# Performance work log

Measured on AMD Instinct MI355X. Metric: run time of the kernel, lower is better.

Reference implementation:

```python
import jax, jax.numpy as jnp
import numpy as np

ALPHA = 0.5  # config_param['alpha']


def setup_inputs() -> dict:
    key = jax.random.key(0)
    ks = jax.random.split(key, 10)
    B, T, N, E, H = 64, 20, 8192, 128, 128
    # sparse multi-hot basket indicators
    x = (jax.random.uniform(ks[0], (B, T, N)) < 0.01).astype(jnp.float32)
    seq_len = jax.random.randint(ks[1], (B,), 1, T + 1)  # pack_padded requires >=1
    A = jax.random.uniform(ks[2], (N, N), dtype=jnp.float32) * 0.01  # dense item-item adjacency
    W1 = jax.random.normal(ks[3], (E, N), dtype=jnp.float32) * 0.02
    b1 = jnp.zeros((E,), jnp.float32)
    W2 = jax.random.normal(ks[4], (E, N), dtype=jnp.float32) * 0.02
    b2 = jnp.zeros((E,), jnp.float32)
    W_ih = jax.random.normal(ks[5], (4 * H, E), dtype=jnp.float32) * 0.05
    W_hh = jax.random.normal(ks[6], (4 * H, H), dtype=jnp.float32) * 0.05
    b_ih = jnp.zeros((4 * H,), jnp.float32)
    b_hh = jnp.zeros((4 * H,), jnp.float32)
    W_out = jax.random.normal(ks[7], (N, H), dtype=jnp.float32) * 0.02
    I_B = jnp.ones((N,), jnp.float32) / N  # item_probs-style bias init
    threshold = jnp.array([0.005], jnp.float32)  # adj_matrix.mean()
    return dict(x=x, seq_len=seq_len, A=A, W1=W1, b1=b1, W2=W2, b2=b2,
                W_ih=W_ih, W_hh=W_hh, b_ih=b_ih, b_hh=b_hh,
                W_out=W_out, I_B=I_B, threshold=threshold)


def reference(x, seq_len, A, W1, b1, W2, b2, W_ih, W_hh, b_ih, b_hh, W_out, I_B, threshold):
    B, T, N = x.shape
    H = W_hh.shape[1]
    xf = x.reshape(B * T, N)
    # two basket encoders, elementwise max combine (dropout = identity in eval)
    e1 = jax.nn.relu(xf @ W1.T + b1)
    e2 = jax.nn.relu(xf @ W2.T + b2)
    basket = jnp.maximum(e1, e2).reshape(B, T, -1)  # [B, T, E]

    # 1-layer LSTM (torch gate order i,f,g,o); packed variable-length seqs
    # emulated by freezing (h, c) once t >= seq_len, so h_n matches pack_padded.
    valid = jnp.arange(T)[:, None] < seq_len[None, :]  # [T, B]
    xs = basket.transpose(1, 0, 2)                     # [T, B, E]
    b = b_ih + b_hh

    def step(carry, inp):
        h, c = carry
        x_t, v = inp
        gates = x_t @ W_ih.T + h @ W_hh.T + b
        i, f, g, o = jnp.split(gates, 4, axis=-1)
        c_new = jax.nn.sigmoid(f) * c + jax.nn.sigmoid(i) * jnp.tanh(g)
        h_new = jax.nn.sigmoid(o) * jnp.tanh(c_new)
        m = v[:, None]
        return (jnp.where(m, h_new, h), jnp.where(m, c_new, c)), None

    h0 = jnp.zeros((B, H), x.dtype)
    c0 = jnp.zeros((B, H), x.dtype)
    (h_n, _), _ = jax.lax.scan(step, (h0, c0), (xs, valid))

    p = jax.nn.sigmoid(h_n @ W_out.T)  # [B, N]
    # mm(p, diag(relu(I_B))) is algebraically an elementwise scale
    predict = (1.0 - ALPHA) * p + ALPHA * (p * jax.nn.relu(I_B) + jax.nn.relu(p @ A))
    return predict
```

## Files before the change

kernel.cpp:

```cpp
#include <hip/hip_runtime.h>
#include <hip/hip_bf16.h>
#include <stdint.h>

#define B_ 64
#define T_ 20
#define N_ 8192
#define E_ 128
#define H_ 128
#define G4 512
#define SPLITK 16

typedef short bf16x8 __attribute__((ext_vector_type(8)));
typedef float f32x4 __attribute__((ext_vector_type(4)));

__device__ __forceinline__ float sigmoidf_(float x){ return 1.0f/(1.0f+expf(-x)); }

__device__ __forceinline__ unsigned short f2bf(float f){
  union { float f; uint32_t u; } v; v.f = f;
  uint32_t u = v.u;
  uint32_t r = (u + 0x7FFFu + ((u >> 16) & 1u)) >> 16;
  return (unsigned short)r;
}
__device__ __forceinline__ uint32_t pk2(float a, float b){
  return (uint32_t)f2bf(a) | ((uint32_t)f2bf(b) << 16);
}
__device__ __forceinline__ float bf2f(unsigned short s){
  union { uint32_t u; float f; } v; v.u = ((uint32_t)s) << 16; return v.f;
}

__global__ void k_transpose(const float* __restrict__ W1, const float* __restrict__ W2,
                            float* __restrict__ W12T){
  __shared__ float t1[128][33];
  __shared__ float t2[128][33];
  int n0 = blockIdx.x * 32;
  int tid = threadIdx.x;
  int nl = tid & 31, eg = tid >> 5;
  for (int i = 0; i < 16; i++){
    int e = eg * 16 + i;
    t1[e][nl] = W1[(size_t)e*N_ + n0 + nl];
    t2[e][nl] = W2[(size_t)e*N_ + n0 + nl];
  }
  __syncthreads();
  for (int n = 0; n < 32; n++){
    float v = (tid < 128) ? t1[tid][n] : t2[tid-128][n];
    W12T[(size_t)(n0+n)*256 + tid] = v;
  }
}

__global__ void k_mlpx(const float* __restrict__ x, const int* __restrict__ seq_len,
                       const float* __restrict__ W12T, const float* __restrict__ b1,
                       const float* __restrict__ b2, const float* __restrict__ W_ih,
                       const float* __restrict__ b_ih, const float* __restrict__ b_hh,
                       float* __restrict__ Xp){
  int bt = blockIdx.x;
  int b = bt / T_, t = bt % T_;
  if (t >= seq_len[b]) return;
  __shared__ int idxs[1024];
  __shared__ int cnt;
  __shared__ float e2s[128];
  __shared__ float bx[128];
  int tid = threadIdx.x;
  if (tid == 0) cnt = 0;
  __syncthreads();
  const float4* xr = (const float4*)(x + (size_t)bt * N_);
  for (int i = 0; i < 8; i++){
    float4 v = xr[i*256 + tid];
    int base = (i*256 + tid)*4;
    if (v.x != 0.f){ int q = atomicAdd(&cnt,1); idxs[q] = base;   }
    if (v.y != 0.f){ int q = atomicAdd(&cnt,1); idxs[q] = base+1; }
    if (v.z != 0.f){ int q = atomicAdd(&cnt,1); idxs[q] = base+2; }
    if (v.w != 0.f){ int q = atomicAdd(&cnt,1); idxs[q] = base+3; }
  }
  __syncthreads();
  int m = cnt; if (m > 1024) m = 1024;
  float acc = (tid < 128) ? b1[tid] : b2[tid-128];
  for (int i = 0; i < m; i++)
    acc += W12T[(size_t)idxs[i]*256 + tid];
  acc = fmaxf(acc, 0.f);
  if (tid >= 128) e2s[tid-128] = acc;
  __syncthreads();
  if (tid < 128) bx[tid] = fmaxf(acc, e2s[tid]);
  __syncthreads();
  #pragma unroll
  for (int half = 0; half < 2; half++){
    int j = half*256 + tid;
    const float4* wr = (const float4*)(W_ih + (size_t)j * E_);
    float s0 = b_ih[j] + b_hh[j], s1 = 0.f, s2 = 0.f, s3 = 0.f;
    #pragma unroll
    for (int k4 = 0; k4 < 32; k4 += 4){
      float4 w, h;
      w = wr[k4+0]; h = *(const float4*)&bx[k4*4+ 0]; s0 += w.x*h.x + w.y*h.y + w.z*h.z + w.w*h.w;
      w = wr[k4+1]; h = *(const float4*)&bx[k4*4+ 4]; s1 += w.x*h.x + w.y*h.y + w.z*h.z + w.w*h.w;
      w = wr[k4+2]; h = *(const float4*)&bx[k4*4+ 8]; s2 += w.x*h.x + w.y*h.y + w.z*h.z + w.w*h.w;
      w = wr[k4+3]; h = *(const float4*)&bx[k4*4+12]; s3 += w.x*h.x + w.y*h.y + w.z*h.z + w.w*h.w;
    }
    Xp[(size_t)bt*G4 + j] = (s0 + s1) + (s2 + s3);
  }
}

__global__ void __launch_bounds__(512, 2)
k_lstm(const int* __restrict__ seq_len, const float* __restrict__ Xp,
       const float* __restrict__ W_hh, float* __restrict__ hn){
  int b = blockIdx.x;
  int L = seq_len[b];
  int j = threadIdx.x;
  float4 whh[32];
  const float4* wr = (const float4*)(W_hh + (size_t)j * H_);
  #pragma unroll
  for (int k = 0; k < 32; k++) whh[k] = wr[k];
  __shared__ float hs[128];
  __shared__ float gs[512];
  if (j < 128) hs[j] = 0.f;
  float c = 0.f;
  __syncthreads();
  for (int t = 0; t < L; t++){
    float s0 = Xp[((size_t)b*T_ + t)*G4 + j], s1 = 0.f, s2 = 0.f, s3 = 0.f;
    #pragma unroll
    for (int k = 0; k < 32; k += 4){
      float4 w, h;
      w = whh[k+0]; h = *(const float4*)&hs[k*4+ 0]; s0 += w.x*h.x + w.y*h.y + w.z*h.z + w.w*h.w;
      w = whh[k+1]; h = *(const float4*)&hs[k*4+ 4]; s1 += w.x*h.x + w.y*h.y + w.z*h.z + w.w*h.w;
      w = whh[k+2]; h = *(const float4*)&hs[k*4+ 8]; s2 += w.x*h.x + w.y*h.y + w.z*h.z + w.w*h.w;
      w = whh[k+3]; h = *(const float4*)&hs[k*4+12]; s3 += w.x*h.x + w.y*h.y + w.z*h.z + w.w*h.w;
    }
    gs[j] = (s0 + s1) + (s2 + s3);
    __syncthreads();
    if (j < 128){
      float i_ = gs[j], f_ = gs[128+j], gg = gs[256+j], o_ = gs[384+j];
      c = sigmoidf_(f_)*c + sigmoidf_(i_)*tanhf(gg);
      hs[j] = sigmoidf_(o_)*tanhf(c);
    }
    __syncthreads();
  }
  if (j < 128) hn[(size_t)b*H_ + j] = hs[j];
}

__global__ void k_pout(const float* __restrict__ hn, const float* __restrict__ W_out,
                       unsigned short* __restrict__ pbf){
  __shared__ unsigned short hb[64*128];
  int tid = threadIdx.x;
  {
    int row = tid >> 2;
    int k16 = (tid & 3) * 32;
    const float4* hr = (const float4*)(hn + (size_t)row*H_ + k16);
    #pragma unroll
    for (int i = 0; i < 4; i++){
      float4 a = hr[i*2], bq = hr[i*2+1];
      uint4 u; u.x = pk2(a.x,a.y); u.y = pk2(a.z,a.w); u.z = pk2(bq.x,bq.y); u.w = pk2(bq.z,bq.w);
      int blk = (k16 >> 3) + i;
      *(uint4*)&hb[row*128 + ((blk ^ (row & 7)) * 8)] = u;
    }
  }
  __syncthreads();
  int w = tid >> 6, l = tid & 63;
  int n0 = blockIdx.x * 128;
  f32x4 acc[8];
  #pragma unroll
  for (int i = 0; i < 8; i++) acc[i] = (f32x4){0.f,0.f,0.f,0.f};
  int row = w*16 + (l & 15);
  #pragma unroll
  for (int ks = 0; ks < 4; ks++){
    int kk = ks*32 + (l >> 4)*8;
    int blk = kk >> 3;
    bf16x8 af = *(bf16x8*)&hb[row*128 + ((blk ^ (row & 7)) * 8)];
    #pragma unroll
    for (int nt = 0; nt < 8; nt++){
      int n = n0 + nt*16 + (l & 15);
      const float4* wp = (const float4*)(W_out + (size_t)n*H_ + kk);
      float4 wa = wp[0], wb = wp[1];
      union { uint4 u; bf16x8 v; } cc;
      cc.u.x = pk2(wa.x,wa.y); cc.u.y = pk2(wa.z,wa.w);
      cc.u.z = pk2(wb.x,wb.y); cc.u.w = pk2(wb.z,wb.w);
      acc[nt] = __builtin_amdgcn_mfma_f32_16x16x32_bf16(af, cc.v, acc[nt], 0, 0, 0);
    }
  }
  #pragma unroll
  for (int nt = 0; nt < 8; nt++){
    int n = n0 + nt*16 + (l & 15);
    #pragma unroll
    for (int r = 0; r < 4; r++){
      int rr = w*16 + (l >> 4)*4 + r;
      float pv = 1.f/(1.f + expf(-acc[nt][r]));
      pbf[(size_t)rr*N_ + n] = f2bf(pv);
    }
  }
}

__global__ void __launch_bounds__(256, 3)
k_gemm(const unsigned short* __restrict__ pbf, const float* __restrict__ Ag,
       float* __restrict__ Cp){
  __shared__ unsigned short Abf[2][128*32];
  __shared__ unsigned short pt[2][64*32];
  int tid = threadIdx.x;
  int nb = blockIdx.x & 63, ks = blockIdx.x >> 6;
  int n0 = nb * 128;
  int kbase = ks * (N_ / SPLITK);
  int w = tid >> 6, l = tid & 63;
  f32x4 acc[8];
  #pragma unroll
  for (int i = 0; i < 8; i++) acc[i] = (f32x4){0.f,0.f,0.f,0.f};
  int sn = tid & 127, kq = tid >> 7;
  int prow = tid >> 2, phw = (tid & 3) * 8;
  float* Cout = Cp + (size_t)ks * (B_ * N_);
  const int NSTEP = (N_ / SPLITK) / 32;

  float aA[16], aB[16];
  uint4 pA, pB;

  auto issue = [&](float* ar, uint4& pr, int kb) {
    pr = *(const uint4*)&pbf[(size_t)prow*N_ + kb + phw];
    #pragma unroll
    for (int i = 0; i < 4; i++){
      int k4 = kq*16 + i*4;
      const float* base = Ag + (size_t)(kb + k4)*N_ + n0 + sn;
      ar[i*4+0] = __builtin_nontemporal_load(base);
      ar[i*4+1] = __builtin_nontemporal_load(base + (size_t)N_);
      ar[i*4+2] = __builtin_nontemporal_load(base + (size_t)2*N_);
      ar[i*4+3] = __builtin_nontemporal_load(base + (size_t)3*N_);
    }
  };
  auto stage = [&](int buf, const float* ar, const uint4& pr) {
    *(uint4*)&pt[buf][prow*32 + phw] = pr;
    #pragma unroll
    for (int i = 0; i < 4; i++){
      int k4 = kq*16 + i*4;
      uint2 u; u.x = pk2(ar[i*4+0], ar[i*4+1]); u.y = pk2(ar[i*4+2], ar[i*4+3]);
      *(uint2*)&Abf[buf][sn*32 + (k4 ^ ((sn & 3) * 8))] = u;
    }
  };
  auto compute = [&](int buf) {
    bf16x8 af = *(bf16x8*)&pt[buf][(w*16 + (l & 15))*32 + (l >> 4)*8];
    #pragma unroll
    for (int nt = 0; nt < 8; nt++){
      int n = nt*16 + (l & 15);
      bf16x8 bfr = *(bf16x8*)&Abf[buf][n*32 + (((l >> 4)*8) ^ ((n & 3)*8))];
      acc[nt] = __builtin_amdgcn_mfma_f32_16x16x32_bf16(af, bfr, acc[nt], 0, 0, 0);
    }
  };

  issue(aA, pA, kbase);
  for (int s = 0; s < NSTEP; s += 2){
    if (s + 1 < NSTEP) issue(aB, pB, kbase + (s+1)*32);
    stage(0, aA, pA);
    asm volatile("s_waitcnt lgkmcnt(0)" ::: "memory");
    __builtin_amdgcn_sched_barrier(0);
    __builtin_amdgcn_s_barrier();
    __builtin_amdgcn_sched_barrier(0);
    compute(0);
    if (s + 2 < NSTEP) issue(aA, pA, kbase + (s+2)*32);
    stage(1, aB, pB);
    asm volatile("s_waitcnt lgkmcnt(0)" ::: "memory");
    __builtin_amdgcn_sched_barrier(0);
    __builtin_amdgcn_s_barrier();
    __builtin_amdgcn_sched_barrier(0);
    compute(1);
  }

  #pragma unroll
  for (int nt = 0; nt < 8; nt++){
    int n = n0 + nt*16 + (l & 15);
    #pragma unroll
    for (int r = 0; r < 4; r++){
      int rr = w*16 + (l >> 4)*4 + r;
      Cout[(size_t)rr*N_ + n] = acc[nt][r];
    }
  }
}

__global__ void k_final(const unsigned short* __restrict__ pbf, const float* __restrict__ Cp,
                        const float* __restrict__ I_B, float* __restrict__ out){
  int idx = blockIdx.x*256 + threadIdx.x;
  ushort4 pu = ((const ushort4*)pbf)[idx];
  float4 cv = {0.f, 0.f, 0.f, 0.f};
  #pragma unroll
  for (int s = 0; s < SPLITK; s++){
    float4 v = ((const float4*)(Cp + (size_t)s * (B_ * N_)))[idx];
    cv.x += v.x; cv.y += v.y; cv.z += v.z; cv.w += v.w;
  }
  int n = (idx*4) & (N_-1);
  float4 ib = *(const float4*)&I_B[n];
  float4 o;
  float p0 = bf2f(pu.x), p1 = bf2f(pu.y), p2 = bf2f(pu.z), p3 = bf2f(pu.w);
  o.x = 0.5f*p0 + 0.5f*(p0*fmaxf(ib.x,0.f) + fmaxf(cv.x,0.f));
  o.y = 0.5f*p1 + 0.5f*(p1*fmaxf(ib.y,0.f) + fmaxf(cv.y,0.f));
  o.z = 0.5f*p2 + 0.5f*(p2*fmaxf(ib.z,0.f) + fmaxf(cv.z,0.f));
  o.w = 0.5f*p3 + 0.5f*(p3*fmaxf(ib.w,0.f) + fmaxf(cv.w,0.f));
  ((float4*)out)[idx] = o;
}

extern "C" void kernel_launch(void* const* d_in, const int* in_sizes, int n_in,
                              void* d_out, int out_size, void* d_ws, size_t ws_size,
                              hipStream_t stream) {
  const float* x     = (const float*)d_in[0];
  const int*   seq   = (const int*)  d_in[1];
  const float* A     = (const float*)d_in[2];
  const float* W1    = (const float*)d_in[3];
  const float* b1    = (const float*)d_in[4];
  const float* W2    = (const float*)d_in[5];
  const float* b2    = (const float*)d_in[6];
  const float* W_ih  = (const float*)d_in[7];
  const float* W_hh  = (const float*)d_in[8];
  const float* b_ih  = (const float*)d_in[9];
  const float* b_hh  = (const float*)d_in[10];
  const float* W_out = (const float*)d_in[11];
  const float* I_B   = (const float*)d_in[12];
  float* out = (float*)d_out;

  float* ws     = (float*)d_ws;
  float* W12T   = ws;
  float* Xp     = W12T + 2097152;
  float* hn     = Xp + 655360;
  float* Cp     = hn + 8192;
  unsigned short* pbf = (unsigned short*)(Cp + 8388608);

  k_transpose<<<256, 256, 0, stream>>>(W1, W2, W12T);
  k_mlpx     <<<1280,256, 0, stream>>>(x, seq, W12T, b1, b2, W_ih, b_ih, b_hh, Xp);
  k_lstm     <<<64,  512, 0, stream>>>(seq, Xp, W_hh, hn);
  k_pout     <<<64,  256, 0, stream>>>(hn, W_out, pbf);
  k_gemm     <<<64*SPLITK, 256, 0, stream>>>(pbf, A, Cp);
  k_final    <<<512, 256, 0, stream>>>(pbf, Cp, I_B, out);
}
```

Before: 175.1 us.

## Fuse all stages into one cooperative persistent kernel with grid syncs

Replaces the six separate kernel launches with a single cooperative kernel of 256 blocks x 512 threads that moves between the transpose, basket encoder, LSTM, output projection, p@A GEMM and final combine using grid.sync(). It also lowers split-K from 16 to 4 and retiles the GEMM with 64-wide K steps and a 2x2 MFMA tile per wave, which shrinks the partial-sum buffer and the final reduction. The basket encoder now caps nonzero indices at 256 per row and splits the gather across two thread halves. The aim is to cut launch gaps and partial-sum traffic. In exchange, the GEMM runs on only 256 blocks with lower occupancy, and most blocks sit idle during the LSTM and projection phases.

```diff
diff --git a/kernel.cpp b/kernel.cpp
--- a/kernel.cpp
+++ b/kernel.cpp
@@ -1,6 +1,8 @@
 #include <hip/hip_runtime.h>
-#include <hip/hip_bf16.h>
+#include <hip/hip_cooperative_groups.h>
 #include <stdint.h>
+
+namespace cg = cooperative_groups;
 
 #define B_ 64
 #define T_ 20
@@ -8,7 +10,7 @@
 #define E_ 128
 #define H_ 128
 #define G4 512
-#define SPLITK 16
+#define SPLITK 4
 
 typedef short bf16x8 __attribute__((ext_vector_type(8)));
 typedef float f32x4 __attribute__((ext_vector_type(4)));
@@ -28,264 +30,299 @@
   union { uint32_t u; float f; } v; v.u = ((uint32_t)s) << 16; return v.f;
 }
 
-__global__ void k_transpose(const float* __restrict__ W1, const float* __restrict__ W2,
-                            float* __restrict__ W12T){
-  __shared__ float t1[128][33];
-  __shared__ float t2[128][33];
-  int n0 = blockIdx.x * 32;
-  int tid = threadIdx.x;
-  int nl = tid & 31, eg = tid >> 5;
-  for (int i = 0; i < 16; i++){
-    int e = eg * 16 + i;
-    t1[e][nl] = W1[(size_t)e*N_ + n0 + nl];
-    t2[e][nl] = W2[(size_t)e*N_ + n0 + nl];
-  }
-  __syncthreads();
-  for (int n = 0; n < 32; n++){
-    float v = (tid < 128) ? t1[tid][n] : t2[tid-128][n];
-    W12T[(size_t)(n0+n)*256 + tid] = v;
-  }
-}
-
-__global__ void k_mlpx(const float* __restrict__ x, const int* __restrict__ seq_len,
-                       const float* __restrict__ W12T, const float* __restrict__ b1,
-                       const float* __restrict__ b2, const float* __restrict__ W_ih,
-                       const float* __restrict__ b_ih, const float* __restrict__ b_hh,
-                       float* __restrict__ Xp){
-  int bt = blockIdx.x;
-  int b = bt / T_, t = bt % T_;
-  if (t >= seq_len[b]) return;
-  __shared__ int idxs[1024];
-  __shared__ int cnt;
-  __shared__ float e2s[128];
-  __shared__ float bx[128];
-  int tid = threadIdx.x;
-  if (tid == 0) cnt = 0;
-  __syncthreads();
-  const float4* xr = (const float4*)(x + (size_t)bt * N_);
-  for (int i = 0; i < 8; i++){
-    float4 v = xr[i*256 + tid];
-    int base = (i*256 + tid)*4;
-    if (v.x != 0.f){ int q = atomicAdd(&cnt,1); idxs[q] = base;   }
-    if (v.y != 0.f){ int q = atomicAdd(&cnt,1); idxs[q] = base+1; }
-    if (v.z != 0.f){ int q = atomicAdd(&cnt,1); idxs[q] = base+2; }
-    if (v.w != 0.f){ int q = atomicAdd(&cnt,1); idxs[q] = base+3; }
-  }
-  __syncthreads();
-  int m = cnt; if (m > 1024) m = 1024;
-  float acc = (tid < 128) ? b1[tid] : b2[tid-128];
-  for (int i = 0; i < m; i++)
-    acc += W12T[(size_t)idxs[i]*256 + tid];
-  acc = fmaxf(acc, 0.f);
-  if (tid >= 128) e2s[tid-128] = acc;
-  __syncthreads();
-  if (tid < 128) bx[tid] = fmaxf(acc, e2s[tid]);
-  __syncthreads();
-  #pragma unroll
-  for (int half = 0; half < 2; half++){
-    int j = half*256 + tid;
-    const float4* wr = (const float4*)(W_ih + (size_t)j * E_);
-    float s0 = b_ih[j] + b_hh[j], s1 = 0.f, s2 = 0.f, s3 = 0.f;
-    #pragma unroll
-    for (int k4 = 0; k4 < 32; k4 += 4){
-      float4 w, h;
-      w = wr[k4+0]; h = *(const float4*)&bx[k4*4+ 0]; s0 += w.x*h.x + w.y*h.y + w.z*h.z + w.w*h.w;
-      w = wr[k4+1]; h = *(const float4*)&bx[k4*4+ 4]; s1 += w.x*h.x + w.y*h.y + w.z*h.z + w.w*h.w;
-      w = wr[k4+2]; h = *(const float4*)&bx[k4*4+ 8]; s2 += w.x*h.x + w.y*h.y + w.z*h.z + w.w*h.w;
-      w = wr[k4+3]; h = *(const float4*)&bx[k4*4+12]; s3 += w.x*h.x + w.y*h.y + w.z*h.z + w.w*h.w;
-    }
-    Xp[(size_t)bt*G4 + j] = (s0 + s1) + (s2 + s3);
-  }
-}
-
 __global__ void __launch_bounds__(512, 2)
-k_lstm(const int* __restrict__ seq_len, const float* __restrict__ Xp,
-       const float* __restrict__ W_hh, float* __restrict__ hn){
-  int b = blockIdx.x;
-  int L = seq_len[b];
-  int j = threadIdx.x;
-  float4 whh[32];
-  const float4* wr = (const float4*)(W_hh + (size_t)j * H_);
-  #pragma unroll
-  for (int k = 0; k < 32; k++) whh[k] = wr[k];
-  __shared__ float hs[128];
-  __shared__ float gs[512];
-  if (j < 128) hs[j] = 0.f;
-  float c = 0.f;
-  __syncthreads();
-  for (int t = 0; t < L; t++){
-    float s0 = Xp[((size_t)b*T_ + t)*G4 + j], s1 = 0.f, s2 = 0.f, s3 = 0.f;
-    #pragma unroll
-    for (int k = 0; k < 32; k += 4){
-      float4 w, h;
-      w = whh[k+0]; h = *(const float4*)&hs[k*4+ 0]; s0 += w.x*h.x + w.y*h.y + w.z*h.z + w.w*h.w;
-      w = whh[k+1]; h = *(const float4*)&hs[k*4+ 4]; s1 += w.x*h.x + w.y*h.y + w.z*h.z + w.w*h.w;
-      w = whh[k+2]; h = *(const float4*)&hs[k*4+ 8]; s2 += w.x*h.x + w.y*h.y + w.z*h.z + w.w*h.w;
-      w = whh[k+3]; h = *(const float4*)&hs[k*4+12]; s3 += w.x*h.x + w.y*h.y + w.z*h.z + w.w*h.w;
-    }
-    gs[j] = (s0 + s1) + (s2 + s3);
+mega(const float* __restrict__ x, const int* __restrict__ seq_len,
+     const float* __restrict__ Ag, const float* __restrict__ W1,
+     const float* __restrict__ b1, const float* __restrict__ W2,
+     const float* __restrict__ b2, const float* __restrict__ W_ih,
+     const float* __restrict__ W_hh, const float* __restrict__ b_ih,
+     const float* __restrict__ b_hh, const float* __restrict__ W_out,
+     const float* __restrict__ I_B, float* __restrict__ out,
+     float* __restrict__ W12T, float* __restrict__ Xp,
+     float* __restrict__ hn, float* __restrict__ Cp,
+     unsigned short* __restrict__ pbf){
+  __shared__ char smem_raw[49152] __attribute__((aligned(16)));
+  cg::grid_group grid = cg::this_grid();
+  const int blk = blockIdx.x;
+  const int tid = threadIdx.x;
+
+  {
+    float (*t1)[33] = (float(*)[33])smem_raw;
+    float (*t2)[33] = (float(*)[33])(smem_raw + 128*33*4);
+    int n0 = blk * 32;
+    int nl = tid & 31, eg = tid >> 5;
+    #pragma unroll
+    for (int i = 0; i < 8; i++){
+      int e = eg*8 + i;
+      t1[e][nl] = W1[(size_t)e*N_ + n0 + nl];
+      t2[e][nl] = W2[(size_t)e*N_ + n0 + nl];
+    }
     __syncthreads();
-    if (j < 128){
-      float i_ = gs[j], f_ = gs[128+j], gg = gs[256+j], o_ = gs[384+j];
-      c = sigmoidf_(f_)*c + sigmoidf_(i_)*tanhf(gg);
-      hs[j] = sigmoidf_(o_)*tanhf(c);
-    }
+    int c = tid & 255, hf = tid >> 8;
+    #pragma unroll
+    for (int nn = 0; nn < 16; nn++){
+      int n = hf*16 + nn;
+      float v = (c < 128) ? t1[c][n] : t2[c-128][n];
+      W12T[(size_t)(n0+n)*256 + c] = v;
+    }
+  }
+  grid.sync();
+
+  {
+    int*   idxs = (int*)smem_raw;
+    int*   cntp = idxs + 256;
+    float* sums = (float*)(smem_raw + 1040);
+    float* bx   = sums + 512;
+    int e = tid & 255, hf = tid >> 8;
+    for (int it = 0; it < 5; it++){
+      int bt = it*256 + blk;
+      int b = bt / T_, t = bt % T_;
+      if (t >= seq_len[b]) continue;
+      __syncthreads();
+      if (tid == 0) *cntp = 0;
+      __syncthreads();
+      const float4* xr = (const float4*)(x + (size_t)bt * N_);
+      #pragma unroll
+      for (int i = 0; i < 4; i++){
+        float4 v = xr[i*512 + tid];
+        int base = (i*512 + tid)*4;
+        if (v.x != 0.f) idxs[atomicAdd(cntp,1) & 255] = base;
+        if (v.y != 0.f) idxs[atomicAdd(cntp,1) & 255] = base+1;
+        if (v.z != 0.f) idxs[atomicAdd(cntp,1) & 255] = base+2;
+        if (v.w != 0.f) idxs[atomicAdd(cntp,1) & 255] = base+3;
+      }
+      __syncthreads();
+      int m = *cntp; if (m > 256) m = 256;
+      float acc = (hf == 0) ? ((e < 128) ? b1[e] : b2[e-128]) : 0.f;
+      for (int i = hf; i < m; i += 2)
+        acc += W12T[(size_t)idxs[i]*256 + e];
+      sums[hf*256 + e] = acc;
+      __syncthreads();
+      if (tid < 128){
+        float r0 = fmaxf(sums[tid]     + sums[256+tid], 0.f);
+        float r1 = fmaxf(sums[128+tid] + sums[384+tid], 0.f);
+        bx[tid] = fmaxf(r0, r1);
+      }
+      __syncthreads();
+      const float4* wr = (const float4*)(W_ih + (size_t)tid * E_);
+      float s0 = b_ih[tid] + b_hh[tid], s1 = 0.f, s2 = 0.f, s3 = 0.f;
+      #pragma unroll
+      for (int k4 = 0; k4 < 32; k4 += 4){
+        float4 w, h;
+        w = wr[k4+0]; h = *(const float4*)&bx[k4*4+ 0]; s0 += w.x*h.x + w.y*h.y + w.z*h.z + w.w*h.w;
+        w = wr[k4+1]; h = *(const float4*)&bx[k4*4+ 4]; s1 += w.x*h.x + w.y*h.y + w.z*h.z + w.w*h.w;
+        w = wr[k4+2]; h = *(const float4*)&bx[k4*4+ 8]; s2 += w.x*h.x + w.y*h.y + w.z*h.z + w.w*h.w;
+        w = wr[k4+3]; h = *(const float4*)&bx[k4*4+12]; s3 += w.x*h.x + w.y*h.y + w.z*h.z + w.w*h.w;
+      }
+      Xp[(size_t)bt*G4 + tid] = (s0 + s1) + (s2 + s3);
+    }
+  }
+  grid.sync();
+
+  if (blk < 64){
+    float* hs = (float*)smem_raw;
+    float* gs = hs + 128;
+    int L = seq_len[blk];
+    int j = tid;
+    float4 whh[32];
+    const float4* wr = (const float4*)(W_hh + (size_t)j * H_);
+    #pragma unroll
+    for (int k = 0; k < 32; k++) whh[k] = wr[k];
+    if (j < 128) hs[j] = 0.f;
+    float c = 0.f;
     __syncthreads();
-  }
-  if (j < 128) hn[(size_t)b*H_ + j] = hs[j];
-}
-
-__global__ void k_pout(const float* __restrict__ hn, const float* __restrict__ W_out,
-                       unsigned short* __restrict__ pbf){
-  __shared__ unsigned short hb[64*128];
-  int tid = threadIdx.x;
+    for (int t = 0; t < L; t++){
+      float s0 = Xp[((size_t)blk*T_ + t)*G4 + j], s1 = 0.f, s2 = 0.f, s3 = 0.f;
+      #pragma unroll
+      for (int k = 0; k < 32; k += 4){
+        float4 w, h;
+        w = whh[k+0]; h = *(const float4*)&hs[k*4+ 0]; s0 += w.x*h.x + w.y*h.y + w.z*h.z + w.w*h.w;
+        w = whh[k+1]; h = *(const float4*)&hs[k*4+ 4]; s1 += w.x*h.x + w.y*h.y + w.z*h.z + w.w*h.w;
+        w = whh[k+2]; h = *(const float4*)&hs[k*4+ 8]; s2 += w.x*h.x + w.y*h.y + w.z*h.z + w.w*h.w;
+        w = whh[k+3]; h = *(const float4*)&hs[k*4+12]; s3 += w.x*h.x + w.y*h.y + w.z*h.z + w.w*h.w;
+      }
+      gs[j] = (s0 + s1) + (s2 + s3);
+      __syncthreads();
+      if (j < 128){
+        float i_ = gs[j], f_ = gs[128+j], gg = gs[256+j], o_ = gs[384+j];
+        c = sigmoidf_(f_)*c + sigmoidf_(i_)*tanhf(gg);
+        hs[j] = sigmoidf_(o_)*tanhf(c);
+      }
+      __syncthreads();
+    }
+    if (j < 128) hn[(size_t)blk*H_ + j] = hs[j];
+  }
+  grid.sync();
+
+  if (blk < 64){
+    unsigned short* hb = (unsigned short*)smem_raw;
+    if (tid < 256){
+      int row = tid >> 2;
+      int k16 = (tid & 3) * 32;
+      const float4* hr = (const float4*)(hn + (size_t)row*H_ + k16);
+      #pragma unroll
+      for (int i = 0; i < 4; i++){
+        float4 a = hr[i*2], bq = hr[i*2+1];
+        uint4 u; u.x = pk2(a.x,a.y); u.y = pk2(a.z,a.w); u.z = pk2(bq.x,bq.y); u.w = pk2(bq.z,bq.w);
+        int blkk = (k16 >> 3) + i;
+        *(uint4*)&hb[row*128 + ((blkk ^ (row & 7)) * 8)] = u;
+      }
+    }
+    __syncthreads();
+    if (tid < 256){
+      int w = tid >> 6, l = tid & 63;
+      int n0 = blk * 128;
+      f32x4 acc[8];
+      #pragma unroll
+      for (int i = 0; i < 8; i++) acc[i] = (f32x4){0.f,0.f,0.f,0.f};
+      int row = w*16 + (l & 15);
+      #pragma unroll
+      for (int ks = 0; ks < 4; ks++){
+        int kk = ks*32 + (l >> 4)*8;
+        int blkk = kk >> 3;
+        bf16x8 af = *(bf16x8*)&hb[row*128 + ((blkk ^ (row & 7)) * 8)];
+        #pragma unroll
+        for (int nt = 0; nt < 8; nt++){
+          int n = n0 + nt*16 + (l & 15);
+          const float4* wp = (const float4*)(W_out + (size_t)n*H_ + kk);
+          float4 wa = wp[0], wb = wp[1];
+          union { uint4 u; bf16x8 v; } cc;
+          cc.u.x = pk2(wa.x,wa.y); cc.u.y = pk2(wa.z,wa.w);
+          cc.u.z = pk2(wb.x,wb.y); cc.u.w = pk2(wb.z,wb.w);
+          acc[nt] = __builtin_amdgcn_mfma_f32_16x16x32_bf16(af, cc.v, acc[nt], 0, 0, 0);
+        }
+      }
+      #pragma unroll
+      for (int nt = 0; nt < 8; nt++){
+        int n = n0 + nt*16 + (l & 15);
+        #pragma unroll
+        for (int r = 0; r < 4; r++){
+          int rr = w*16 + (l >> 4)*4 + r;
+          float pv = 1.f/(1.f + expf(-acc[nt][r]));
+          pbf[(size_t)rr*N_ + n] = f2bf(pv);
+        }
+      }
+    }
+  }
+  grid.sync();
+
   {
-    int row = tid >> 2;
-    int k16 = (tid & 3) * 32;
-    const float4* hr = (const float4*)(hn + (size_t)row*H_ + k16);
-    #pragma unroll
-    for (int i = 0; i < 4; i++){
-      float4 a = hr[i*2], bq = hr[i*2+1];
-      uint4 u; u.x = pk2(a.x,a.y); u.y = pk2(a.z,a.w); u.z = pk2(bq.x,bq.y); u.w = pk2(bq.z,bq.w);
-      int blk = (k16 >> 3) + i;
-      *(uint4*)&hb[row*128 + ((blk ^ (row & 7)) * 8)] = u;
-    }
-  }
-  __syncthreads();
-  int w = tid >> 6, l = tid & 63;
-  int n0 = blockIdx.x * 128;
-  f32x4 acc[8];
-  #pragma unroll
-  for (int i = 0; i < 8; i++) acc[i] = (f32x4){0.f,0.f,0.f,0.f};
-  int row = w*16 + (l & 15);
-  #pragma unroll
-  for (int ks = 0; ks < 4; ks++){
-    int kk = ks*32 + (l >> 4)*8;
-    int blk = kk >> 3;
-    bf16x8 af = *(bf16x8*)&hb[row*128 + ((blk ^ (row & 7)) * 8)];
-    #pragma unroll
-    for (int nt = 0; nt < 8; nt++){
-      int n = n0 + nt*16 + (l & 15);
-      const float4* wp = (const float4*)(W_out + (size_t)n*H_ + kk);
-      float4 wa = wp[0], wb = wp[1];
-      union { uint4 u; bf16x8 v; } cc;
-      cc.u.x = pk2(wa.x,wa.y); cc.u.y = pk2(wa.z,wa.w);
-      cc.u.z = pk2(wb.x,wb.y); cc.u.w = pk2(wb.z,wb.w);
-      acc[nt] = __builtin_amdgcn_mfma_f32_16x16x32_bf16(af, cc.v, acc[nt], 0, 0, 0);
-    }
-  }
-  #pragma unroll
-  for (int nt = 0; nt < 8; nt++){
-    int n = n0 + nt*16 + (l & 15);
-    #pragma unroll
-    for (int r = 0; r < 4; r++){
-      int rr = w*16 + (l >> 4)*4 + r;
-      float pv = 1.f/(1.f + expf(-acc[nt][r]));
-      pbf[(size_t)rr*N_ + n] = f2bf(pv);
-    }
-  }
-}
-
-__global__ void __launch_bounds__(256, 3)
-k_gemm(const unsigned short* __restrict__ pbf, const float* __restrict__ Ag,
-       float* __restrict__ Cp){
-  __shared__ unsigned short Abf[2][128*32];
-  __shared__ unsigned short pt[2][64*32];
-  int tid = threadIdx.x;
-  int nb = blockIdx.x & 63, ks = blockIdx.x >> 6;
-  int n0 = nb * 128;
-  int kbase = ks * (N_ / SPLITK);
-  int w = tid >> 6, l = tid & 63;
-  f32x4 acc[8];
-  #pragma unroll
-  for (int i = 0; i < 8; i++) acc[i] = (f32x4){0.f,0.f,0.f,0.f};
-  int sn = tid & 127, kq = tid >> 7;
-  int prow = tid >> 2, phw = (tid & 3) * 8;
-  float* Cout = Cp + (size_t)ks * (B_ * N_);
-  const int NSTEP = (N_ / SPLITK) / 32;
-
-  float aA[16], aB[16];
-  uint4 pA, pB;
-
-  auto issue = [&](float* ar, uint4& pr, int kb) {
-    pr = *(const uint4*)&pbf[(size_t)prow*N_ + kb + phw];
-    #pragma unroll
-    for (int i = 0; i < 4; i++){
-      int k4 = kq*16 + i*4;
-      const float* base = Ag + (size_t)(kb + k4)*N_ + n0 + sn;
-      ar[i*4+0] = __builtin_nontemporal_load(base);
-      ar[i*4+1] = __builtin_nontemporal_load(base + (size_t)N_);
-      ar[i*4+2] = __builtin_nontemporal_load(base + (size_t)2*N_);
-      ar[i*4+3] = __builtin_nontemporal_load(base + (size_t)3*N_);
-    }
-  };
-  auto stage = [&](int buf, const float* ar, const uint4& pr) {
-    *(uint4*)&pt[buf][prow*32 + phw] = pr;
-    #pragma unroll
-    for (int i = 0; i < 4; i++){
-      int k4 = kq*16 + i*4;
-      uint2 u; u.x = pk2(ar[i*4+0], ar[i*4+1]); u.y = pk2(ar[i*4+2], ar[i*4+3]);
-      *(uint2*)&Abf[buf][sn*32 + (k4 ^ ((sn & 3) * 8))] = u;
-    }
-  };
-  auto compute = [&](int buf) {
-    bf16x8 af = *(bf16x8*)&pt[buf][(w*16 + (l & 15))*32 + (l >> 4)*8];
-    #pragma unroll
-    for (int nt = 0; nt < 8; nt++){
-      int n = nt*16 + (l & 15);
-      bf16x8 bfr = *(bf16x8*)&Abf[buf][n*32 + (((l >> 4)*8) ^ ((n & 3)*8))];
-      acc[nt] = __builtin_amdgcn_mfma_f32_16x16x32_bf16(af, bfr, acc[nt], 0, 0, 0);
-    }
-  };
-
-  issue(aA, pA, kbase);
-  for (int s = 0; s < NSTEP; s += 2){
-    if (s + 1 < NSTEP) issue(aB, pB, kbase + (s+1)*32);
-    stage(0, aA, pA);
-    asm volatile("s_waitcnt lgkmcnt(0)" ::: "memory");
-    __builtin_amdgcn_sched_barrier(0);
-    __builtin_amdgcn_s_barrier();
-    __builtin_amdgcn_sched_barrier(0);
-    compute(0);
-    if (s + 2 < NSTEP) issue(aA, pA, kbase + (s+2)*32);
-    stage(1, aB, pB);
-    asm volatile("s_waitcnt lgkmcnt(0)" ::: "memory");
-    __builtin_amdgcn_sched_barrier(0);
-    __builtin_amdgcn_s_barrier();
-    __builtin_amdgcn_sched_barrier(0);
-    compute(1);
-  }
-
-  #pragma unroll
-  for (int nt = 0; nt < 8; nt++){
-    int n = n0 + nt*16 + (l & 15);
-    #pragma unroll
-    for (int r = 0; r < 4; r++){
-      int rr = w*16 + (l >> 4)*4 + r;
-      Cout[(size_t)rr*N_ + n] = acc[nt][r];
-    }
-  }
-}
-
-__global__ void k_final(const unsigned short* __restrict__ pbf, const float* __restrict__ Cp,
-                        const float* __restrict__ I_B, float* __restrict__ out){
-  int idx = blockIdx.x*256 + threadIdx.x;
-  ushort4 pu = ((const ushort4*)pbf)[idx];
-  float4 cv = {0.f, 0.f, 0.f, 0.f};
-  #pragma unroll
-  for (int s = 0; s < SPLITK; s++){
-    float4 v = ((const float4*)(Cp + (size_t)s * (B_ * N_)))[idx];
-    cv.x += v.x; cv.y += v.y; cv.z += v.z; cv.w += v.w;
-  }
-  int n = (idx*4) & (N_-1);
-  float4 ib = *(const float4*)&I_B[n];
-  float4 o;
-  float p0 = bf2f(pu.x), p1 = bf2f(pu.y), p2 = bf2f(pu.z), p3 = bf2f(pu.w);
-  o.x = 0.5f*p0 + 0.5f*(p0*fmaxf(ib.x,0.f) + fmaxf(cv.x,0.f));
-  o.y = 0.5f*p1 + 0.5f*(p1*fmaxf(ib.y,0.f) + fmaxf(cv.y,0.f));
-  o.z = 0.5f*p2 + 0.5f*(p2*fmaxf(ib.z,0.f) + fmaxf(cv.z,0.f));
-  o.w = 0.5f*p3 + 0.5f*(p3*fmaxf(ib.w,0.f) + fmaxf(cv.w,0.f));
-  ((float4*)out)[idx] = o;
+    unsigned short* Abf0 = (unsigned short*)smem_raw;
+    unsigned short* Abf1 = Abf0 + 8192;
+    unsigned short* pt0  = Abf1 + 8192;
+    unsigned short* pt1  = pt0 + 4096;
+    int nb = blk & 63, ks = blk >> 6;
+    int n0 = nb * 128;
+    int kbase = ks * (N_ / SPLITK);
+    int sn = tid & 127, kq = tid >> 7;
+    int prow = tid >> 3, c8 = tid & 7;
+    int w = tid >> 6, l = tid & 63;
+    int wm = w >> 2, wn = w & 3;
+    f32x4 acc[2][2];
+    #pragma unroll
+    for (int i = 0; i < 2; i++)
+      #pragma unroll
+      for (int q = 0; q < 2; q++) acc[i][q] = (f32x4){0.f,0.f,0.f,0.f};
+    float* Cout = Cp + (size_t)ks * (B_ * N_);
+    const int NSTEP = (N_ / SPLITK) / 64;
+
+    float aA[16], aB[16];
+    uint4 pA, pB;
+
+    auto issue = [&](float* ar, uint4& pr, int kb){
+      pr = *(const uint4*)&pbf[(size_t)prow*N_ + kb + c8*8];
+      #pragma unroll
+      for (int i = 0; i < 4; i++){
+        const float* base = Ag + (size_t)(kb + kq*16 + i*4)*N_ + n0 + sn;
+        ar[i*4+0] = base[0];
+        ar[i*4+1] = base[(size_t)N_];
+        ar[i*4+2] = base[(size_t)2*N_];
+        ar[i*4+3] = base[(size_t)3*N_];
+      }
+    };
+    auto stage = [&](unsigned short* abf, unsigned short* ptb, const float* ar, const uint4& pr){
+      *(uint4*)&ptb[prow*64 + ((c8*8) ^ ((prow & 7)*8))] = pr;
+      #pragma unroll
+      for (int i = 0; i < 4; i++){
+        int k = kq*16 + i*4;
+        uint2 u; u.x = pk2(ar[i*4+0], ar[i*4+1]); u.y = pk2(ar[i*4+2], ar[i*4+3]);
+        *(uint2*)&abf[sn*64 + (k ^ ((sn & 7)*8))] = u;
+      }
+    };
+    auto compute = [&](const unsigned short* abf, const unsigned short* ptb){
+      #pragma unroll
+      for (int kc = 0; kc < 64; kc += 32){
+        int ko = kc + (l >> 4)*8;
+        bf16x8 af[2], bfr[2];
+        #pragma unroll
+        for (int mi = 0; mi < 2; mi++){
+          int r = wm*32 + mi*16 + (l & 15);
+          af[mi] = *(const bf16x8*)&ptb[r*64 + (ko ^ ((r & 7)*8))];
+        }
+        #pragma unroll
+        for (int ni = 0; ni < 2; ni++){
+          int n = wn*32 + ni*16 + (l & 15);
+          bfr[ni] = *(const bf16x8*)&abf[n*64 + (ko ^ ((n & 7)*8))];
+        }
+        #pragma unroll
+        for (int mi = 0; mi < 2; mi++)
+          #pragma unroll
+          for (int ni = 0; ni < 2; ni++)
+            acc[mi][ni] = __builtin_amdgcn_mfma_f32_16x16x32_bf16(af[mi], bfr[ni], acc[mi][ni], 0, 0, 0);
+      }
+    };
+
+    issue(aA, pA, kbase);
+    for (int s = 0; s < NSTEP; s += 2){
+      if (s + 1 < NSTEP) issue(aB, pB, kbase + (s+1)*64);
+      stage(Abf0, pt0, aA, pA);
+      asm volatile("s_waitcnt lgkmcnt(0)" ::: "memory");
+      __builtin_amdgcn_sched_barrier(0);
+      __builtin_amdgcn_s_barrier();
+      __builtin_amdgcn_sched_barrier(0);
+      compute(Abf0, pt0);
+      if (s + 2 < NSTEP) issue(aA, pA, kbase + (s+2)*64);
+      stage(Abf1, pt1, aB, pB);
+      asm volatile("s_waitcnt lgkmcnt(0)" ::: "memory");
+      __builtin_amdgcn_sched_barrier(0);
+      __builtin_amdgcn_s_barrier();
+      __builtin_amdgcn_sched_barrier(0);
+      compute(Abf1, pt1);
+    }
+
+    #pragma unroll
+    for (int mi = 0; mi < 2; mi++)
+      #pragma unroll
+      for (int ni = 0; ni < 2; ni++){
+        int n = n0 + wn*32 + ni*16 + (l & 15);
+        #pragma unroll
+        for (int r = 0; r < 4; r++){
+          int rr = wm*32 + mi*16 + (l >> 4)*4 + r;
+          Cout[(size_t)rr*N_ + n] = acc[mi][ni][r];
+        }
+      }
+  }
+  grid.sync();
+
+  {
+    int idx = blk*512 + tid;
+    ushort4 pu = ((const ushort4*)pbf)[idx];
+    float4 cv = {0.f, 0.f, 0.f, 0.f};
+    #pragma unroll
+    for (int s = 0; s < SPLITK; s++){
+      float4 v = ((const float4*)(Cp + (size_t)s * (B_ * N_)))[idx];
+      cv.x += v.x; cv.y += v.y; cv.z += v.z; cv.w += v.w;
+    }
+    int n = (idx*4) & (N_-1);
+    float4 ib = *(const float4*)&I_B[n];
+    float4 o;
+    float p0 = bf2f(pu.x), p1 = bf2f(pu.y), p2 = bf2f(pu.z), p3 = bf2f(pu.w);
+    o.x = 0.5f*p0 + 0.5f*(p0*fmaxf(ib.x,0.f) + fmaxf(cv.x,0.f));
+    o.y = 0.5f*p1 + 0.5f*(p1*fmaxf(ib.y,0.f) + fmaxf(cv.y,0.f));
+    o.z = 0.5f*p2 + 0.5f*(p2*fmaxf(ib.z,0.f) + fmaxf(cv.z,0.f));
+    o.w = 0.5f*p3 + 0.5f*(p3*fmaxf(ib.w,0.f) + fmaxf(cv.w,0.f));
+    ((float4*)out)[idx] = o;
+  }
 }
 
 extern "C" void kernel_launch(void* const* d_in, const int* in_sizes, int n_in,
@@ -306,17 +343,17 @@
   const float* I_B   = (const float*)d_in[12];
   float* out = (float*)d_out;
 
-  float* ws     = (float*)d_ws;
-  float* W12T   = ws;
-  float* Xp     = W12T + 2097152;
-  float* hn     = Xp + 655360;
-  float* Cp     = hn + 8192;
-  unsigned short* pbf = (unsigned short*)(Cp + 8388608);
-
-  k_transpose<<<256, 256, 0, stream>>>(W1, W2, W12T);
-  k_mlpx     <<<1280,256, 0, stream>>>(x, seq, W12T, b1, b2, W_ih, b_ih, b_hh, Xp);
-  k_lstm     <<<64,  512, 0, stream>>>(seq, Xp, W_hh, hn);
-  k_pout     <<<64,  256, 0, stream>>>(hn, W_out, pbf);
-  k_gemm     <<<64*SPLITK, 256, 0, stream>>>(pbf, A, Cp);
-  k_final    <<<512, 256, 0, stream>>>(pbf, Cp, I_B, out);
-}
+  float* ws   = (float*)d_ws;
+  float* W12T = ws;
+  float* Xp   = W12T + 2097152;
+  float* hn   = Xp + 655360;
+  float* Cp   = hn + 8192;
+  unsigned short* pbf = (unsigned short*)(Cp + 2097152);
+
+  void* args[] = {(void*)&x, (void*)&seq, (void*)&A, (void*)&W1, (void*)&b1,
+                  (void*)&W2, (void*)&b2, (void*)&W_ih, (void*)&W_hh,
+                  (void*)&b_ih, (void*)&b_hh, (void*)&W_out, (void*)&I_B,
+                  (void*)&out, (void*)&W12T, (void*)&Xp, (void*)&hn,
+                  (void*)&Cp, (void*)&pbf};
+  hipLaunchCooperativeKernel((void*)mega, dim3(256), dim3(512), args, 0, stream);
+}
```

After: 350.4 us. 100% more time.

## Retile p@A GEMM with 512 threads, K=64 steps, halve split-K, unroll sparse gather

Applied to the files above, without the earlier changes.

The p@A GEMM now runs 512-thread blocks. Each wave owns a 32x32 sub-tile of the 64x128 output, and each stage covers K=64 instead of 32, with XOR-swizzled LDS layouts for both operands. Split-K drops from 16 to 8, which halves the partial-sum buffer that k_final has to write and reduce, but gives fewer blocks. The A loads switch from nontemporal to regular loads. Separately, the sparse embedding gather in k_mlpx is unrolled by 8 so more independent loads are in flight, which slightly changes the float summation order.

```diff
diff --git a/kernel.cpp b/kernel.cpp
--- a/kernel.cpp
+++ b/kernel.cpp
@@ -8,7 +8,7 @@
 #define E_ 128
 #define H_ 128
 #define G4 512
-#define SPLITK 16
+#define SPLITK 8
 
 typedef short bf16x8 __attribute__((ext_vector_type(8)));
 typedef float f32x4 __attribute__((ext_vector_type(4)));
@@ -74,7 +74,21 @@
   __syncthreads();
   int m = cnt; if (m > 1024) m = 1024;
   float acc = (tid < 128) ? b1[tid] : b2[tid-128];
-  for (int i = 0; i < m; i++)
+  int i = 0;
+  for (; i + 8 <= m; i += 8){
+    int j0 = idxs[i+0], j1 = idxs[i+1], j2 = idxs[i+2], j3 = idxs[i+3];
+    int j4 = idxs[i+4], j5 = idxs[i+5], j6 = idxs[i+6], j7 = idxs[i+7];
+    float v0 = W12T[(size_t)j0*256 + tid];
+    float v1 = W12T[(size_t)j1*256 + tid];
+    float v2 = W12T[(size_t)j2*256 + tid];
+    float v3 = W12T[(size_t)j3*256 + tid];
+    float v4 = W12T[(size_t)j4*256 + tid];
+    float v5 = W12T[(size_t)j5*256 + tid];
+    float v6 = W12T[(size_t)j6*256 + tid];
+    float v7 = W12T[(size_t)j7*256 + tid];
+    acc += ((v0+v1)+(v2+v3)) + ((v4+v5)+(v6+v7));
+  }
+  for (; i < m; i++)
     acc += W12T[(size_t)idxs[i]*256 + tid];
   acc = fmaxf(acc, 0.f);
   if (tid >= 128) e2s[tid-128] = acc;
@@ -186,85 +200,104 @@
   }
 }
 
-__global__ void __launch_bounds__(256, 3)
+__global__ void __launch_bounds__(512, 4)
 k_gemm(const unsigned short* __restrict__ pbf, const float* __restrict__ Ag,
        float* __restrict__ Cp){
-  __shared__ unsigned short Abf[2][128*32];
-  __shared__ unsigned short pt[2][64*32];
+  __shared__ unsigned short Abf0[128*64];
+  __shared__ unsigned short Abf1[128*64];
+  __shared__ unsigned short pt0[64*64];
+  __shared__ unsigned short pt1[64*64];
   int tid = threadIdx.x;
   int nb = blockIdx.x & 63, ks = blockIdx.x >> 6;
   int n0 = nb * 128;
   int kbase = ks * (N_ / SPLITK);
+  int sn = tid & 127, kq = tid >> 7;
+  int prow = tid >> 3, c8 = tid & 7;
   int w = tid >> 6, l = tid & 63;
-  f32x4 acc[8];
-  #pragma unroll
-  for (int i = 0; i < 8; i++) acc[i] = (f32x4){0.f,0.f,0.f,0.f};
-  int sn = tid & 127, kq = tid >> 7;
-  int prow = tid >> 2, phw = (tid & 3) * 8;
+  int wm = w >> 2, wn = w & 3;
+  f32x4 acc[2][2];
+  #pragma unroll
+  for (int i = 0; i < 2; i++)
+    #pragma unroll
+    for (int q = 0; q < 2; q++) acc[i][q] = (f32x4){0.f,0.f,0.f,0.f};
   float* Cout = Cp + (size_t)ks * (B_ * N_);
-  const int NSTEP = (N_ / SPLITK) / 32;
+  const int NSTEP = (N_ / SPLITK) / 64;
 
   float aA[16], aB[16];
   uint4 pA, pB;
 
-  auto issue = [&](float* ar, uint4& pr, int kb) {
-    pr = *(const uint4*)&pbf[(size_t)prow*N_ + kb + phw];
+  auto issue = [&](float* ar, uint4& pr, int kb){
+    pr = *(const uint4*)&pbf[(size_t)prow*N_ + kb + c8*8];
     #pragma unroll
     for (int i = 0; i < 4; i++){
-      int k4 = kq*16 + i*4;
-      const float* base = Ag + (size_t)(kb + k4)*N_ + n0 + sn;
-      ar[i*4+0] = __builtin_nontemporal_load(base);
-      ar[i*4+1] = __builtin_nontemporal_load(base + (size_t)N_);
-      ar[i*4+2] = __builtin_nontemporal_load(base + (size_t)2*N_);
-      ar[i*4+3] = __builtin_nontemporal_load(base + (size_t)3*N_);
+      const float* base = Ag + (size_t)(kb + kq*16 + i*4)*N_ + n0 + sn;
+      ar[i*4+0] = base[0];
+      ar[i*4+1] = base[(size_t)N_];
+      ar[i*4+2] = base[(size_t)2*N_];
+      ar[i*4+3] = base[(size_t)3*N_];
     }
   };
-  auto stage = [&](int buf, const float* ar, const uint4& pr) {
-    *(uint4*)&pt[buf][prow*32 + phw] = pr;
+  auto stage = [&](unsigned short* abf, unsigned short* ptb, const float* ar, const uint4& pr){
+    *(uint4*)&ptb[prow*64 + ((c8*8) ^ ((prow & 7)*8))] = pr;
     #pragma unroll
     for (int i = 0; i < 4; i++){
-      int k4 = kq*16 + i*4;
+      int k = kq*16 + i*4;
       uint2 u; u.x = pk2(ar[i*4+0], ar[i*4+1]); u.y = pk2(ar[i*4+2], ar[i*4+3]);
-      *(uint2*)&Abf[buf][sn*32 + (k4 ^ ((sn & 3) * 8))] = u;
+      *(uint2*)&abf[sn*64 + (k ^ ((sn & 7)*8))] = u;
     }
   };
-  auto compute = [&](int buf) {
-    bf16x8 af = *(bf16x8*)&pt[buf][(w*16 + (l & 15))*32 + (l >> 4)*8];
-    #pragma unroll
-    for (int nt = 0; nt < 8; nt++){
-      int n = nt*16 + (l & 15);
-      bf16x8 bfr = *(bf16x8*)&Abf[buf][n*32 + (((l >> 4)*8) ^ ((n & 3)*8))];
-      acc[nt] = __builtin_amdgcn_mfma_f32_16x16x32_bf16(af, bfr, acc[nt], 0, 0, 0);
+  auto compute = [&](const unsigned short* abf, const unsigned short* ptb){
+    #pragma unroll
+    for (int kc = 0; kc < 64; kc += 32){
+      int ko = kc + (l >> 4)*8;
+      bf16x8 af[2], bfr[2];
+      #pragma unroll
+      for (int mi = 0; mi < 2; mi++){
+        int r = wm*32 + mi*16 + (l & 15);
+        af[mi] = *(const bf16x8*)&ptb[r*64 + (ko ^ ((r & 7)*8))];
+      }
+      #pragma unroll
+      for (int ni = 0; ni < 2; ni++){
+        int n = wn*32 + ni*16 + (l & 15);
+        bfr[ni] = *(const bf16x8*)&abf[n*64 + (ko ^ ((n & 7)*8))];
+      }
+      #pragma unroll
+      for (int mi = 0; mi < 2; mi++)
+        #pragma unroll
+        for (int ni = 0; ni < 2; ni++)
+          acc[mi][ni] = __builtin_amdgcn_mfma_f32_16x16x32_bf16(af[mi], bfr[ni], acc[mi][ni], 0, 0, 0);
     }
   };
 
   issue(aA, pA, kbase);
   for (int s = 0; s < NSTEP; s += 2){
-    if (s + 1 < NSTEP) issue(aB, pB, kbase + (s+1)*32);
-    stage(0, aA, pA);
+    if (s + 1 < NSTEP) issue(aB, pB, kbase + (s+1)*64);
+    stage(Abf0, pt0, aA, pA);
     asm volatile("s_waitcnt lgkmcnt(0)" ::: "memory");
     __builtin_amdgcn_sched_barrier(0);
     __builtin_amdgcn_s_barrier();
     __builtin_amdgcn_sched_barrier(0);
-    compute(0);
-    if (s + 2 < NSTEP) issue(aA, pA, kbase + (s+2)*32);
-    stage(1, aB, pB);
+    compute(Abf0, pt0);
+    if (s + 2 < NSTEP) issue(aA, pA, kbase + (s+2)*64);
+    stage(Abf1, pt1, aB, pB);
     asm volatile("s_waitcnt lgkmcnt(0)" ::: "memory");
     __builtin_amdgcn_sched_barrier(0);
     __builtin_amdgcn_s_barrier();
     __builtin_amdgcn_sched_barrier(0);
-    compute(1);
-  }
-
-  #pragma unroll
-  for (int nt = 0; nt < 8; nt++){
-    int n = n0 + nt*16 + (l & 15);
-    #pragma unroll
-    for (int r = 0; r < 4; r++){
-      int rr = w*16 + (l >> 4)*4 + r;
-      Cout[(size_t)rr*N_ + n] = acc[nt][r];
-    }
-  }
+    compute(Abf1, pt1);
+  }
+
+  #pragma unroll
+  for (int mi = 0; mi < 2; mi++)
+    #pragma unroll
+    for (int ni = 0; ni < 2; ni++){
+      int n = n0 + wn*32 + ni*16 + (l & 15);
+      #pragma unroll
+      for (int r = 0; r < 4; r++){
+        int rr = wm*32 + mi*16 + (l >> 4)*4 + r;
+        Cout[(size_t)rr*N_ + n] = acc[mi][ni][r];
+      }
+    }
 }
 
 __global__ void k_final(const unsigned short* __restrict__ pbf, const float* __restrict__ Cp,
@@ -306,17 +339,17 @@
   const float* I_B   = (const float*)d_in[12];
   float* out = (float*)d_out;
 
-  float* ws     = (float*)d_ws;
-  float* W12T   = ws;
-  float* Xp     = W12T + 2097152;
-  float* hn     = Xp + 655360;
-  float* Cp     = hn + 8192;
-  unsigned short* pbf = (unsigned short*)(Cp + 8388608);
+  float* ws   = (float*)d_ws;
+  float* W12T = ws;
+  float* Xp   = W12T + 2097152;
+  float* hn   = Xp + 655360;
+  float* Cp   = hn + 8192;
+  unsigned short* pbf = (unsigned short*)(Cp + 4194304);
 
   k_transpose<<<256, 256, 0, stream>>>(W1, W2, W12T);
   k_mlpx     <<<1280,256, 0, stream>>>(x, seq, W12T, b1, b2, W_ih, b_ih, b_hh, Xp);
   k_lstm     <<<64,  512, 0, stream>>>(seq, Xp, W_hh, hn);
   k_pout     <<<64,  256, 0, stream>>>(hn, W_out, pbf);
-  k_gemm     <<<64*SPLITK, 256, 0, stream>>>(pbf, A, Cp);
+  k_gemm     <<<64*SPLITK, 512, 0, stream>>>(pbf, A, Cp);
   k_final    <<<512, 256, 0, stream>>>(pbf, Cp, I_B, out);
 }
```

New measurement: 177.7 us. No clear change (+1.5%).
